# Performance work log

Measured on AMD Instinct MI355X. Metric: run time of the kernel, lower is better.

The kernel has to match this reference:

```python
import jax, jax.numpy as jnp
import numpy as np

B, S, D_MODEL = 1, 2048, 4096
N_HEADS, N_KV_HEADS = 32, 8
HEAD_DIM = D_MODEL // N_HEADS  # 128
N_REP = N_HEADS // N_KV_HEADS  # 4
ROPE_THETA = 500000.0
NEG_INF = -1e9


def setup_inputs() -> dict:
    key = jax.random.key(0)
    ks = jax.random.split(key, 6)
    std = 0.02 * (2 * 32) ** (-0.5)
    x = jax.random.normal(ks[0], (B, S, D_MODEL), dtype=jnp.float32)
    wq = jax.random.normal(ks[1], (N_HEADS * HEAD_DIM, D_MODEL), dtype=jnp.float32) * std
    wk = jax.random.normal(ks[2], (N_KV_HEADS * HEAD_DIM, D_MODEL), dtype=jnp.float32) * std
    wv = jax.random.normal(ks[3], (N_KV_HEADS * HEAD_DIM, D_MODEL), dtype=jnp.float32) * std
    wo = jax.random.normal(ks[4], (D_MODEL, N_HEADS * HEAD_DIM), dtype=jnp.float32) * std
    cache_k = jnp.zeros((B, S, N_KV_HEADS, HEAD_DIM), dtype=jnp.float32)
    cache_v = jnp.zeros((B, S, N_KV_HEADS, HEAD_DIM), dtype=jnp.float32)
    # RoPE tables: freqs_cis[t, j] = exp(i * t * theta^(-2j/head_dim)), j < head_dim/2
    inv_freq = 1.0 / (ROPE_THETA ** (jnp.arange(0, HEAD_DIM, 2, dtype=jnp.float32) / HEAD_DIM))
    t = jnp.arange(S, dtype=jnp.float32)
    ang = jnp.outer(t, inv_freq)  # [S, HEAD_DIM/2]
    freqs_cos = jnp.cos(ang)
    freqs_sin = jnp.sin(ang)
    # causal additive mask [1, 1, S, S]
    mask = jnp.triu(jnp.full((S, S), NEG_INF, dtype=jnp.float32), k=1)[None, None]
    return {"x": x, "wq": wq, "wk": wk, "wv": wv, "wo": wo,
            "cache_k": cache_k, "cache_v": cache_v,
            "freqs_cos": freqs_cos, "freqs_sin": freqs_sin,
            "mask": mask, "start_pos": 0}


def _apply_rope(x, cos, sin):
    # x: [B, S, H, D]; cos/sin: [S, D/2]; pairs (x[2j], x[2j+1]) form complex numbers
    b, s, h, d = x.shape
    x2 = x.astype(jnp.float32).reshape(b, s, h, d // 2, 2)
    xr, xi = x2[..., 0], x2[..., 1]
    c = cos[None, :, None, :]
    sn = sin[None, :, None, :]
    out_r = xr * c - xi * sn
    out_i = xr * sn + xi * c
    return jnp.stack([out_r, out_i], axis=-1).reshape(b, s, h, d)


def reference(x, wq, wk, wv, wo, cache_k, cache_v, freqs_cos, freqs_sin, mask, start_pos):
    bsz, seq_len, _ = x.shape
    xq = (x @ wq.T).reshape(bsz, seq_len, N_HEADS, HEAD_DIM)
    xk = (x @ wk.T).reshape(bsz, seq_len, N_KV_HEADS, HEAD_DIM)
    xv = (x @ wv.T).reshape(bsz, seq_len, N_KV_HEADS, HEAD_DIM)
    xq = _apply_rope(xq, freqs_cos, freqs_sin)
    xk = _apply_rope(xk, freqs_cos, freqs_sin)
    # KV-cache update then read back the valid prefix
    cache_k = jax.lax.dynamic_update_slice(cache_k, xk, (0, start_pos, 0, 0))
    cache_v = jax.lax.dynamic_update_slice(cache_v, xv, (0, start_pos, 0, 0))
    keys = cache_k[:, : start_pos + seq_len]      # [B, K, KVH, D]
    values = cache_v[:, : start_pos + seq_len]
    # repeat_kv: expand kv heads to match query heads
    keys = jnp.repeat(keys, N_REP, axis=2)        # [B, K, H, D]
    values = jnp.repeat(values, N_REP, axis=2)
    q = xq.transpose(0, 2, 1, 3)                  # [B, H, S, D]
    k = keys.transpose(0, 2, 1, 3)                # [B, H, K, D]
    v = values.transpose(0, 2, 1, 3)
    scores = jnp.einsum('bhqd,bhkd->bhqk', q, k) / jnp.float32(np.sqrt(HEAD_DIM))
    scores = scores + mask
    probs = jax.nn.softmax(scores.astype(jnp.float32), axis=-1).astype(q.dtype)
    out = jnp.einsum('bhqk,bhkd->bhqd', probs, v)           # [B, H, S, D]
    out = out.transpose(0, 2, 1, 3).reshape(bsz, seq_len, -1)
    return out @ wo.T
```

## Files before the change

### kernel.cpp

```cpp
#include <hip/hip_runtime.h>
#include <cstdint>
#include <cstddef>

typedef __attribute__((ext_vector_type(8))) short  short8;
typedef __attribute__((ext_vector_type(4))) float  floatx4;
typedef __attribute__((ext_vector_type(4))) unsigned short ushort4v;

__device__ __forceinline__ unsigned short f2b(float f) {
  unsigned u = __builtin_bit_cast(unsigned, f);
  u = u + 0x7fffu + ((u >> 16) & 1u);
  return (unsigned short)(u >> 16);
}
__device__ __forceinline__ float b2f(unsigned short h) {
  unsigned u = ((unsigned)h) << 16;
  return __builtin_bit_cast(float, u);
}

__device__ __forceinline__ void gld_lds16(const void* g, void* l) {
  __builtin_amdgcn_global_load_lds(
      (const __attribute__((address_space(1))) unsigned int*)g,
      (__attribute__((address_space(3))) unsigned int*)l,
      16, 0, 0);
}

__global__ void __launch_bounds__(256) f2b_kernel(const float* __restrict__ in,
                                                  unsigned short* __restrict__ out,
                                                  int n4) {
  int i = blockIdx.x * 256 + threadIdx.x;
  if (i >= n4) return;
  floatx4 v = ((const floatx4*)in)[i];
  ushort4v o;
  o[0] = f2b(v[0]); o[1] = f2b(v[1]); o[2] = f2b(v[2]); o[3] = f2b(v[3]);
  ((ushort4v*)out)[i] = o;
}

template <int MODE>
__global__ void __launch_bounds__(256) gemm_bt(const unsigned short* __restrict__ A,
                                               const unsigned short* __restrict__ B,
                                               float* __restrict__ Cf,
                                               unsigned short* __restrict__ Cb,
                                               int M, int N, int K,
                                               const float* __restrict__ fc,
                                               const float* __restrict__ fs) {
  __shared__ __align__(16) unsigned short As[4096];
  __shared__ __align__(16) unsigned short Bs[4096];
  const int m0 = blockIdx.x * 128;
  const int n0 = blockIdx.y * 128;
  const int tid  = threadIdx.x;
  const int wave = tid >> 6, lane = tid & 63;
  const int quad = lane >> 4, l15 = lane & 15;
  const int wm = ((wave >> 1) & 1) * 64;
  const int wn = (wave & 1) * 64;

  floatx4 acc[4][4] = {};

  const int lr = lane >> 2, sj = lane & 3;
  const unsigned short* pa[2];
  const unsigned short* pb[2];
  unsigned short *la[2], *lb[2];
#pragma unroll
  for (int t = 0; t < 2; ++t) {
    const int i = wave * 2 + t;
    const int r = i * 16 + lr;
    const int o = (sj - (r >> 1)) & 3;
    pa[t] = A + (size_t)(m0 + r) * K + o * 8;
    pb[t] = B + (size_t)(n0 + r) * K + o * 8;
    la[t] = &As[i * 512];
    lb[t] = &Bs[i * 512];
  }

  for (int kt = 0; kt < K; kt += 32) {
    gld_lds16(pa[0] + kt, la[0]);
    gld_lds16(pa[1] + kt, la[1]);
    gld_lds16(pb[0] + kt, lb[0]);
    gld_lds16(pb[1] + kt, lb[1]);
    __syncthreads();

    short8 af[4], bfr[4];
#pragma unroll
    for (int t = 0; t < 4; ++t) {
      const int rA = wm + t * 16 + l15;
      const int ja = (quad + (rA >> 1)) & 3;
      af[t] = *(const short8*)&As[rA * 32 + ja * 8];
      const int rB = wn + t * 16 + l15;
      const int jb = (quad + (rB >> 1)) & 3;
      bfr[t] = *(const short8*)&Bs[rB * 32 + jb * 8];
    }
#pragma unroll
    for (int tm = 0; tm < 4; ++tm)
#pragma unroll
      for (int tn = 0; tn < 4; ++tn)
        acc[tm][tn] = __builtin_amdgcn_mfma_f32_16x16x32_bf16(af[tm], bfr[tn], acc[tm][tn], 0, 0, 0);
    __syncthreads();
  }

#pragma unroll
  for (int tm = 0; tm < 4; ++tm) {
#pragma unroll
    for (int tn = 0; tn < 4; ++tn) {
      const int colb = n0 + wn + tn * 16;
      const int col  = colb + l15;
      const bool rope = (MODE == 2) && (colb < 5120);
      const int p = (col & 127) >> 1;
      const float sgn = (l15 & 1) ? 1.f : -1.f;
#pragma unroll
      for (int r = 0; r < 4; ++r) {
        const int row = m0 + wm + tm * 16 + quad * 4 + r;
        float v = acc[tm][tn][r];
        if (rope) {
          const float partner = __shfl_xor(v, 1);
          const float c  = fc[row * 64 + p];
          const float sn = fs[row * 64 + p];
          v = v * c + partner * sn * sgn;
        }
        if (MODE == 1) Cf[(size_t)row * N + col] = v;
        else           Cb[(size_t)row * N + col] = f2b(v);
      }
    }
  }
}

__global__ void __launch_bounds__(256) transpose_bf16(const unsigned short* __restrict__ in,
                                                      unsigned short* __restrict__ out,
                                                      int R, int C, int in_stride) {
  __shared__ __align__(16) unsigned short tile[64][72];
  const int br = blockIdx.y * 64;
  const int bc = blockIdx.x * 64;
  const int tid = threadIdx.x;
  const int lr = tid >> 3;
  const int lc = (tid & 7) * 8;
#pragma unroll
  for (int it = 0; it < 2; ++it) {
    const int r = it * 32 + lr;
    *(short8*)&tile[r][lc] = *(const short8*)(in + (size_t)(br + r) * in_stride + bc + lc);
  }
  __syncthreads();
#pragma unroll
  for (int it = 0; it < 2; ++it) {
    const int c = it * 32 + lr;
    short8 v;
#pragma unroll
    for (int j = 0; j < 8; ++j) v[j] = (short)tile[lc + j][c];
    *(short8*)(out + (size_t)(bc + c) * R + br + lc) = v;
  }
}

#define SL2E 0.1275500406721347f

__global__ void __launch_bounds__(256) flash_attn(const unsigned short* __restrict__ Q,
                                                  const unsigned short* __restrict__ Kp,
                                                  const unsigned short* __restrict__ Vt,
                                                  unsigned short* __restrict__ O) {
  constexpr int QS = 6144;
  const int bx  = blockIdx.x;
  const int h   = blockIdx.y;
  const int kvh = h >> 2;
  const int tid = threadIdx.x;
  const int wave = tid >> 6, lane = tid & 63;
  const int quad = lane >> 4, l15 = lane & 15;

  __shared__ __align__(16) unsigned short Ks[2][8192];
  __shared__ __align__(16) unsigned short Vs[2][8192];
  __shared__ __align__(16) unsigned short Ps[4][16 * 76];
  unsigned short* Pw = Ps[wave];

  const int i0 = wave * 4;
  const unsigned short* kbase = Kp + kvh * 128;
  const unsigned short* vbase[4];
  int vslot_sc[4];
#pragma unroll
  for (int ii = 0; ii < 4; ++ii) {
    const int i = i0 + ii;
    const int slot = i * 64 + lane;
    const int sc = slot >> 7, d = slot & 127;
    vbase[ii] = Vt + (size_t)(kvh * 128 + d) * 2048;
    vslot_sc[ii] = sc * 8;
  }

  for (int seg = 0; seg < 2; ++seg) {
    const int qt  = seg ? (31 - bx) : bx;
    const int q0  = qt * 64;
    const int qra = q0 + wave * 16;
    const int n   = qt + 1;

    short8 aq[4];
#pragma unroll
    for (int ks = 0; ks < 4; ++ks)
      aq[ks] = *(const short8*)(Q + (size_t)(qra + l15) * QS + h * 128 + ks * 32 + quad * 8);

    floatx4 oacc[8] = {};
    float mrow[4], lrow[4];
#pragma unroll
    for (int r = 0; r < 4; ++r) { mrow[r] = -1e30f; lrow[r] = 0.f; }

    {
      const int cc = 0;
#pragma unroll
      for (int ii = 0; ii < 4; ++ii) {
        const int i = i0 + ii;
        gld_lds16(kbase + (size_t)(cc + lane) * QS + i * 8, &Ks[0][i * 512]);
        gld_lds16(vbase[ii] + cc + vslot_sc[ii], &Vs[0][i * 512]);
      }
    }

    for (int j = 0; j < n; ++j) {
      __syncthreads();
      if (j + 1 < n) {
        const int cc = (j + 1) * 64;
        const int nb = (j + 1) & 1;
#pragma unroll
        for (int ii = 0; ii < 4; ++ii) {
          const int i = i0 + ii;
          gld_lds16(kbase + (size_t)(cc + lane) * QS + i * 8, &Ks[nb][i * 512]);
          gld_lds16(vbase[ii] + cc + vslot_sc[ii], &Vs[nb][i * 512]);
        }
      }
      const unsigned short* kb = Ks[j & 1];
      const unsigned short* vb = Vs[j & 1];
      const int c0 = j * 64;

      floatx4 sacc[4] = {};
#pragma unroll
      for (int ks = 0; ks < 4; ++ks) {
#pragma unroll
        for (int tn = 0; tn < 4; ++tn) {
          short8 bk = *(const short8*)&kb[((ks * 4 + quad) * 64 + tn * 16 + l15) * 8];
          sacc[tn] = __builtin_amdgcn_mfma_f32_16x16x32_bf16(aq[ks], bk, sacc[tn], 0, 0, 0);
        }
      }

      const bool needmask = (c0 + 63 > qra);
#pragma unroll
      for (int r = 0; r < 4; ++r) {
        const int rowg = qra + quad * 4 + r;
        float t0 = sacc[0][r] * SL2E, t1 = sacc[1][r] * SL2E;
        float t2 = sacc[2][r] * SL2E, t3 = sacc[3][r] * SL2E;
        if (needmask) {
          t0 = (c0 +  0 + l15 <= rowg) ? t0 : -1e30f;
          t1 = (c0 + 16 + l15 <= rowg) ? t1 : -1e30f;
          t2 = (c0 + 32 + l15 <= rowg) ? t2 : -1e30f;
          t3 = (c0 + 48 + l15 <= rowg) ? t3 : -1e30f;
        }
        float mx = fmaxf(fmaxf(t0, t1), fmaxf(t2, t3));
#pragma unroll
        for (int off = 1; off < 16; off <<= 1)
          mx = fmaxf(mx, __shfl_xor(mx, off, 16));
        const float mold = mrow[r];
        const float mn   = fmaxf(mold, mx);
        const float alpha = exp2f(mold - mn);
        float p0 = exp2f(t0 - mn), p1 = exp2f(t1 - mn);
        float p2 = exp2f(t2 - mn), p3 = exp2f(t3 - mn);
        sacc[0][r] = p0; sacc[1][r] = p1; sacc[2][r] = p2; sacc[3][r] = p3;
        float lsum = (p0 + p1) + (p2 + p3);
#pragma unroll
        for (int off = 1; off < 16; off <<= 1)
          lsum += __shfl_xor(lsum, off, 16);
        mrow[r] = mn;
        lrow[r] = lrow[r] * alpha + lsum;
#pragma unroll
        for (int tn = 0; tn < 8; ++tn) oacc[tn][r] *= alpha;
      }

#pragma unroll
      for (int tn = 0; tn < 4; ++tn)
#pragma unroll
        for (int r = 0; r < 4; ++r)
          Pw[(quad * 4 + r) * 76 + tn * 16 + l15] = f2b(sacc[tn][r]);

      short8 ap[2];
#pragma unroll
      for (int k2 = 0; k2 < 2; ++k2)
        ap[k2] = *(const short8*)&Pw[l15 * 76 + k2 * 32 + quad * 8];
#pragma unroll
      for (int k2 = 0; k2 < 2; ++k2) {
#pragma unroll
        for (int tn = 0; tn < 8; ++tn) {
          short8 bv = *(const short8*)&vb[((k2 * 4 + quad) * 128 + tn * 16 + l15) * 8];
          oacc[tn] = __builtin_amdgcn_mfma_f32_16x16x32_bf16(ap[k2], bv, oacc[tn], 0, 0, 0);
        }
      }
    }

#pragma unroll
    for (int r = 0; r < 4; ++r) {
      const float inv = 1.f / lrow[r];
      const int rowg = qra + quad * 4 + r;
#pragma unroll
      for (int tn = 0; tn < 8; ++tn)
        O[(size_t)rowg * 4096 + h * 128 + tn * 16 + l15] = f2b(oacc[tn][r] * inv);
    }
    __syncthreads();
  }
}

extern "C" void kernel_launch(void* const* d_in, const int* in_sizes, int n_in,
                              void* d_out, int out_size, void* d_ws, size_t ws_size,
                              hipStream_t stream) {
  const float* x  = (const float*)d_in[0];
  const float* wq = (const float*)d_in[1];
  const float* wk = (const float*)d_in[2];
  const float* wv = (const float*)d_in[3];
  const float* wo = (const float*)d_in[4];
  const float* fc = (const float*)d_in[7];
  const float* fs = (const float*)d_in[8];
  float* out = (float*)d_out;

  char* ws = (char*)d_ws;
  unsigned short* xb    = (unsigned short*)(ws + 0);
  unsigned short* wqkvb = (unsigned short*)(ws + 16777216);
  unsigned short* wob   = (unsigned short*)(ws + 67108864);
  unsigned short* qkv   = (unsigned short*)(ws + 100663296);
  unsigned short* vt    = (unsigned short*)(ws + 125829120);
  unsigned short* ob    = (unsigned short*)(ws + 130023424);
  unsigned short* wkb = wqkvb + (size_t)4096 * 4096;
  unsigned short* wvb = wkb + (size_t)1024 * 4096;

  f2b_kernel<<<8192,  256, 0, stream>>>(x,  xb,    2097152);
  f2b_kernel<<<16384, 256, 0, stream>>>(wq, wqkvb, 4194304);
  f2b_kernel<<<4096,  256, 0, stream>>>(wk, wkb,   1048576);
  f2b_kernel<<<4096,  256, 0, stream>>>(wv, wvb,   1048576);
  f2b_kernel<<<16384, 256, 0, stream>>>(wo, wob,   4194304);

  gemm_bt<2><<<dim3(16, 48), 256, 0, stream>>>(xb, wqkvb, nullptr, qkv, 2048, 6144, 4096, fc, fs);

  transpose_bf16<<<dim3(16, 32), 256, 0, stream>>>(qkv + 5120, vt, 2048, 1024, 6144);

  flash_attn<<<dim3(16, 32), 256, 0, stream>>>(qkv, qkv + 4096, vt, ob);

  gemm_bt<1><<<dim3(16, 32), 256, 0, stream>>>(ob, wob, out, nullptr, 2048, 4096, 4096, nullptr, nullptr);
}
```

Baseline: 640.6 us.

## Replace GEMMs with 256-row double-buffered tiles, XOR swizzle and XCD-aware block mapping

Replaces the 128x128, BK=32 single-buffered GEMM with a 512-thread kernel using 256xBN tiles (BN=192 for QKV, 128 for output), BK=64, and double-buffered LDS. The next tile's global-to-LDS loads are issued while MFMAs run on the current buffer, with barriers and setprio interleaved. Block indices are remapped so neighbouring tiles land on the same XCD for better L2 reuse, and LDS uses an XOR swizzle. This targets load latency and the low arithmetic intensity of the two projection GEMMs, at the cost of more registers and LDS per block and heavier barrier use.

```diff
diff --git a/kernel.cpp b/kernel.cpp
--- a/kernel.cpp
+++ b/kernel.cpp
@@ -10,10 +10,6 @@
   unsigned u = __builtin_bit_cast(unsigned, f);
   u = u + 0x7fffu + ((u >> 16) & 1u);
   return (unsigned short)(u >> 16);
-}
-__device__ __forceinline__ float b2f(unsigned short h) {
-  unsigned u = ((unsigned)h) << 16;
-  return __builtin_bit_cast(float, u);
 }
 
 __device__ __forceinline__ void gld_lds16(const void* g, void* l) {
@@ -34,83 +30,141 @@
   ((ushort4v*)out)[i] = o;
 }
 
-template <int MODE>
-__global__ void __launch_bounds__(256) gemm_bt(const unsigned short* __restrict__ A,
-                                               const unsigned short* __restrict__ B,
-                                               float* __restrict__ Cf,
-                                               unsigned short* __restrict__ Cb,
-                                               int M, int N, int K,
-                                               const float* __restrict__ fc,
-                                               const float* __restrict__ fs) {
-  __shared__ __align__(16) unsigned short As[4096];
-  __shared__ __align__(16) unsigned short Bs[4096];
-  const int m0 = blockIdx.x * 128;
-  const int n0 = blockIdx.y * 128;
+template <int MODE, int BN>
+__global__ void __launch_bounds__(512, 2)
+gemm256(const unsigned short* __restrict__ A,
+        const unsigned short* __restrict__ B,
+        float* __restrict__ Cf,
+        unsigned short* __restrict__ Cb,
+        int K, int N,
+        const float* __restrict__ fc,
+        const float* __restrict__ fs) {
+  constexpr int BM = 256, BK = 64;
+  constexpr int NF  = BN / 64;
+  constexpr int WNC = BN / 4;
+  constexpr int NB  = BN / 64;
+
+  __shared__ __align__(16) unsigned short As[2][BM * BK];
+  __shared__ __align__(16) unsigned short Bs[2][BN * BK];
+
   const int tid  = threadIdx.x;
   const int wave = tid >> 6, lane = tid & 63;
   const int quad = lane >> 4, l15 = lane & 15;
-  const int wm = ((wave >> 1) & 1) * 64;
-  const int wn = (wave & 1) * 64;
-
-  floatx4 acc[4][4] = {};
-
-  const int lr = lane >> 2, sj = lane & 3;
-  const unsigned short* pa[2];
-  const unsigned short* pb[2];
-  unsigned short *la[2], *lb[2];
-#pragma unroll
-  for (int t = 0; t < 2; ++t) {
-    const int i = wave * 2 + t;
-    const int r = i * 16 + lr;
-    const int o = (sj - (r >> 1)) & 3;
-    pa[t] = A + (size_t)(m0 + r) * K + o * 8;
-    pb[t] = B + (size_t)(n0 + r) * K + o * 8;
-    la[t] = &As[i * 512];
-    lb[t] = &Bs[i * 512];
-  }
-
-  for (int kt = 0; kt < K; kt += 32) {
-    gld_lds16(pa[0] + kt, la[0]);
-    gld_lds16(pa[1] + kt, la[1]);
-    gld_lds16(pb[0] + kt, lb[0]);
-    gld_lds16(pb[1] + kt, lb[1]);
-    __syncthreads();
-
-    short8 af[4], bfr[4];
-#pragma unroll
-    for (int t = 0; t < 4; ++t) {
-      const int rA = wm + t * 16 + l15;
-      const int ja = (quad + (rA >> 1)) & 3;
-      af[t] = *(const short8*)&As[rA * 32 + ja * 8];
-      const int rB = wn + t * 16 + l15;
-      const int jb = (quad + (rB >> 1)) & 3;
-      bfr[t] = *(const short8*)&Bs[rB * 32 + jb * 8];
-    }
-#pragma unroll
-    for (int tm = 0; tm < 4; ++tm)
-#pragma unroll
-      for (int tn = 0; tn < 4; ++tn)
-        acc[tm][tn] = __builtin_amdgcn_mfma_f32_16x16x32_bf16(af[tm], bfr[tn], acc[tm][tn], 0, 0, 0);
-    __syncthreads();
-  }
-
-#pragma unroll
-  for (int tm = 0; tm < 4; ++tm) {
-#pragma unroll
-    for (int tn = 0; tn < 4; ++tn) {
-      const int colb = n0 + wn + tn * 16;
+  const int wr = wave >> 2, wc = wave & 3;
+
+  int flat = blockIdx.y * 8 + blockIdx.x;
+  const int cpx = (int)(gridDim.x * gridDim.y) >> 3;
+  flat = (flat & 7) * cpx + (flat >> 3);
+  const int m0 = (flat & 7) * BM;
+  const int n0 = (flat >> 3) * BN;
+
+  const int srow = lane >> 3;
+  const int soct = (lane & 7) ^ srow;
+  const unsigned short* pa[4];
+  const unsigned short* pb[NB];
+#pragma unroll
+  for (int i = 0; i < 4; ++i)
+    pa[i] = A + (size_t)(m0 + wave * 32 + i * 8 + srow) * K + soct * 8;
+#pragma unroll
+  for (int i = 0; i < NB; ++i)
+    pb[i] = B + (size_t)(n0 + wave * (BN / 8) + i * 8 + srow) * K + soct * 8;
+
+  const int xr = l15 & 7;
+  int aoff[2], boff[2];
+#pragma unroll
+  for (int ks = 0; ks < 2; ++ks) {
+    const int sl = ((ks * 4 + quad) ^ xr) * 8;
+    aoff[ks] = (wr * 128 + l15) * 64 + sl;
+    boff[ks] = (wc * WNC + l15) * 64 + sl;
+  }
+
+  floatx4 acc[8][NF] = {};
+  const int NT = K >> 6;
+
+#pragma unroll
+  for (int i = 0; i < 4; ++i)
+    gld_lds16(pa[i], &As[0][(wave * 32 + i * 8) * 64]);
+#pragma unroll
+  for (int i = 0; i < NB; ++i)
+    gld_lds16(pb[i], &Bs[0][(wave * (BN / 8) + i * 8) * 64]);
+  asm volatile("s_waitcnt vmcnt(0)" ::: "memory");
+  __builtin_amdgcn_s_barrier();
+  __builtin_amdgcn_sched_barrier(0);
+
+  int t = 0, kt = 0;
+
+#define TILE_STEP(BUF)                                                         \
+  do {                                                                         \
+          \
+    short8 bfr[NF][2], afr[2][2];                                              \
+    _Pragma("unroll") for (int n = 0; n < NF; ++n)                             \
+      _Pragma("unroll") for (int ks = 0; ks < 2; ++ks)                         \
+        bfr[n][ks] = *(const short8*)&Bs[BUF][boff[ks] + n * 1024];            \
+    _Pragma("unroll") for (int mm = 0; mm < 2; ++mm)                           \
+      _Pragma("unroll") for (int ks = 0; ks < 2; ++ks)                         \
+        afr[mm][ks] = *(const short8*)&As[BUF][aoff[ks] + mm * 1024];          \
+    if (t + 1 < NT) {                                                          \
+      const int kn = kt + 64;                                                  \
+      _Pragma("unroll") for (int i = 0; i < 4; ++i)                            \
+        gld_lds16(pa[i] + kn, &As[1 - (BUF)][(wave * 32 + i * 8) * 64]);       \
+      _Pragma("unroll") for (int i = 0; i < NB; ++i)                           \
+        gld_lds16(pb[i] + kn, &Bs[1 - (BUF)][(wave * (BN / 8) + i * 8) * 64]); \
+    }                                                                          \
+    __builtin_amdgcn_s_barrier();                                              \
+    __builtin_amdgcn_s_setprio(1);                                             \
+    _Pragma("unroll") for (int mm = 0; mm < 2; ++mm)                           \
+      _Pragma("unroll") for (int n = 0; n < NF; ++n)                           \
+        _Pragma("unroll") for (int ks = 0; ks < 2; ++ks)                       \
+          acc[mm][n] = __builtin_amdgcn_mfma_f32_16x16x32_bf16(                \
+              afr[mm][ks], bfr[n][ks], acc[mm][n], 0, 0, 0);                   \
+    __builtin_amdgcn_s_setprio(0);                                             \
+    __builtin_amdgcn_s_barrier();                                              \
+                               \
+    _Pragma("unroll") for (int p = 1; p < 4; ++p) {                            \
+      short8 a2[2][2];                                                         \
+      _Pragma("unroll") for (int mm = 0; mm < 2; ++mm)                         \
+        _Pragma("unroll") for (int ks = 0; ks < 2; ++ks)                       \
+          a2[mm][ks] =                                                         \
+              *(const short8*)&As[BUF][aoff[ks] + (p * 2 + mm) * 1024];        \
+      __builtin_amdgcn_s_barrier();                                            \
+      __builtin_amdgcn_s_setprio(1);                                           \
+      _Pragma("unroll") for (int mm = 0; mm < 2; ++mm)                         \
+        _Pragma("unroll") for (int n = 0; n < NF; ++n)                         \
+          _Pragma("unroll") for (int ks = 0; ks < 2; ++ks)                     \
+            acc[p * 2 + mm][n] = __builtin_amdgcn_mfma_f32_16x16x32_bf16(      \
+                a2[mm][ks], bfr[n][ks], acc[p * 2 + mm][n], 0, 0, 0);          \
+      __builtin_amdgcn_s_setprio(0);                                           \
+      if (p == 3) asm volatile("s_waitcnt vmcnt(0)" ::: "memory");             \
+      __builtin_amdgcn_s_barrier();                                            \
+    }                                                                          \
+    __builtin_amdgcn_sched_barrier(0);                                         \
+    kt += 64;                                                                  \
+    ++t;                                                                       \
+  } while (0)
+
+  while (t < NT) {
+    TILE_STEP(0);
+    TILE_STEP(1);
+  }
+#undef TILE_STEP
+
+#pragma unroll
+  for (int mi = 0; mi < 8; ++mi) {
+#pragma unroll
+    for (int n = 0; n < NF; ++n) {
+      const int colb = n0 + wc * WNC + n * 16;
       const int col  = colb + l15;
       const bool rope = (MODE == 2) && (colb < 5120);
-      const int p = (col & 127) >> 1;
+      const int pp = (col & 127) >> 1;
       const float sgn = (l15 & 1) ? 1.f : -1.f;
 #pragma unroll
       for (int r = 0; r < 4; ++r) {
-        const int row = m0 + wm + tm * 16 + quad * 4 + r;
-        float v = acc[tm][tn][r];
+        const int row = m0 + wr * 128 + mi * 16 + quad * 4 + r;
+        float v = acc[mi][n][r];
         if (rope) {
           const float partner = __shfl_xor(v, 1);
-          const float c  = fc[row * 64 + p];
-          const float sn = fs[row * 64 + p];
+          const float c  = fc[row * 64 + pp];
+          const float sn = fs[row * 64 + pp];
           v = v * c + partner * sn * sgn;
         }
         if (MODE == 1) Cf[(size_t)row * N + col] = v;
@@ -321,11 +375,13 @@
   f2b_kernel<<<4096,  256, 0, stream>>>(wv, wvb,   1048576);
   f2b_kernel<<<16384, 256, 0, stream>>>(wo, wob,   4194304);
 
-  gemm_bt<2><<<dim3(16, 48), 256, 0, stream>>>(xb, wqkvb, nullptr, qkv, 2048, 6144, 4096, fc, fs);
+  gemm256<2, 192><<<dim3(8, 32), 512, 0, stream>>>(xb, wqkvb, nullptr, qkv,
+                                                   4096, 6144, fc, fs);
 
   transpose_bf16<<<dim3(16, 32), 256, 0, stream>>>(qkv + 5120, vt, 2048, 1024, 6144);
 
   flash_attn<<<dim3(16, 32), 256, 0, stream>>>(qkv, qkv + 4096, vt, ob);
 
-  gemm_bt<1><<<dim3(16, 32), 256, 0, stream>>>(ob, wob, out, nullptr, 2048, 4096, 4096, nullptr, nullptr);
-}
+  gemm256<1, 128><<<dim3(8, 32), 512, 0, stream>>>(ob, wob, out, nullptr,
+                                                   4096, 4096, nullptr, nullptr);
+}
```

Result: no change. 629.9 us (-1.7%).
